# Kernel optimization log

Measured on AMD Instinct MI355X. Metric: run time of the kernel, lower is better.

The kernel has to match this reference:

```python
import jax, jax.numpy as jnp
import numpy as np

N = 50000
LEAKY_SLOPE = 0.2


def gat_layer(x, src, dst, W, a_src, a_dst, bias, concat):
    """PyG-style GATConv (eval mode, self-loops already in src/dst).
    x: [N, Fin]; W: [Fin, H*C]; a_src, a_dst: [H, C]; bias: [H*C] or [C].
    """
    H, C = a_src.shape
    h = (x @ W).reshape(-1, H, C)                      # [N, H, C]
    alpha_src = jnp.einsum('nhc,hc->nh', h, a_src)      # [N, H]
    alpha_dst = jnp.einsum('nhc,hc->nh', h, a_dst)      # [N, H]
    e = jax.nn.leaky_relu(alpha_src[src] + alpha_dst[dst], LEAKY_SLOPE)  # [E, H]
    # scatter-softmax over incoming edges of each destination node
    m = jax.lax.stop_gradient(jax.ops.segment_max(e, dst, num_segments=N))
    e = jnp.exp(e - m[dst])
    denom = jax.ops.segment_sum(e, dst, num_segments=N)  # [N, H]
    alpha = e / (denom[dst] + 1e-16)                     # [E, H]
    msg = h[src] * alpha[:, :, None]                     # [E, H, C]
    out = jax.ops.segment_sum(msg, dst, num_segments=N)  # [N, H, C]
    out = out.reshape(-1, H * C) if concat else out.mean(axis=1)
    return out + bias


def setup_inputs() -> dict:
    key = jax.random.key(0)
    ks = jax.random.split(key, 10)
    Fin, Hd, Hh = 256, 64, 4
    E = 1600000
    x = jax.random.normal(ks[0], (N, Fin), dtype=jnp.float32)
    edge_index = jax.random.randint(ks[1], (2, E), 0, N, dtype=jnp.int64)
    s = 1.0 / np.sqrt(Fin)
    W1 = jax.random.normal(ks[2], (Fin, Hh * Hd), dtype=jnp.float32) * s
    att_src1 = jax.random.normal(ks[3], (Hh, Hd), dtype=jnp.float32) * (1.0 / np.sqrt(Hd))
    att_dst1 = jax.random.normal(ks[4], (Hh, Hd), dtype=jnp.float32) * (1.0 / np.sqrt(Hd))
    b1 = jnp.zeros((Hh * Hd,), dtype=jnp.float32)
    W2 = jax.random.normal(ks[5], (Hh * Hd, Hd), dtype=jnp.float32) * (1.0 / np.sqrt(Hh * Hd))
    att_src2 = jax.random.normal(ks[6], (1, Hd), dtype=jnp.float32) * (1.0 / np.sqrt(Hd))
    att_dst2 = jax.random.normal(ks[7], (1, Hd), dtype=jnp.float32) * (1.0 / np.sqrt(Hd))
    b2 = jnp.zeros((Hd,), dtype=jnp.float32)
    return {"x": x, "edge_index": edge_index, "W1": W1, "att_src1": att_src1,
            "att_dst1": att_dst1, "b1": b1, "W2": W2, "att_src2": att_src2,
            "att_dst2": att_dst2, "b2": b2}


def reference(x, edge_index, W1, att_src1, att_dst1, b1, W2, att_src2, att_dst2, b2):
    # PyG GATConv adds self-loops by default
    loop = jnp.arange(N, dtype=edge_index.dtype)
    src = jnp.concatenate([edge_index[0], loop])
    dst = jnp.concatenate([edge_index[1], loop])
    h = gat_layer(x, src, dst, W1, att_src1, att_dst1, b1, concat=True)
    h = jax.nn.elu(h)            # dropout is identity in eval mode
    out = gat_layer(h, src, dst, W2, att_src2, att_dst2, b2, concat=False)
    return out
```

## Files before the change

### kernel.cpp

```cpp
#include <hip/hip_runtime.h>


typedef __attribute__((ext_vector_type(8))) short short8;
typedef __attribute__((ext_vector_type(4))) float floatx4;

#define FIN 256
#define H1 4
#define CH 64
#define CAP 16384

__device__ __forceinline__ float bf2f(ushort u) {
    union { unsigned int i; float f; } v; v.i = ((unsigned int)u) << 16; return v.f;
}
__device__ __forceinline__ ushort f2bf(float f) {
    union { float f; unsigned int i; } v; v.f = f;
    unsigned int r = v.i + 0x7fffu + ((v.i >> 16) & 1u);
    return (ushort)(r >> 16);
}
__device__ __forceinline__ float load_in(const void* p, int i, int f) {
    return f ? ((const float*)p)[i] : bf2f(((const ushort*)p)[i]);
}
__device__ __forceinline__ int load_idx(const void* p, long long i, int f64) {
    return f64 ? (int)((const long long*)p)[i] : ((const int*)p)[i];
}

__global__ __launch_bounds__(256) void probe_kernel(const ushort* __restrict__ x,
                                                    const int* __restrict__ ei,
                                                    int* __restrict__ flags,
                                                    int* __restrict__ bcnt) {
    __shared__ int s_nan, s_odd;
    int t = threadIdx.x;
    bcnt[t] = 0;
    if (t == 0) { s_nan = 0; s_odd = 0; }
    __syncthreads();
    int nanc = 0, oddc = 0;
    for (int i = t; i < 16384; i += 256) {
        ushort u = x[i];
        if (((u >> 7) & 0xFF) == 0xFF) nanc++;
    }
    for (int i = t; i < 2048; i += 256)
        if (ei[2 * i + 1] != 0) oddc++;
    if (nanc) atomicAdd(&s_nan, nanc);
    if (oddc) atomicAdd(&s_odd, oddc);
    __syncthreads();
    if (t == 0) {
        flags[0] = (s_nan >= 2) ? 1 : 0;
        flags[1] = (s_odd == 0) ? 1 : 0;
    }
}

__global__ __launch_bounds__(256) void prep_bucket_kernel(
        const void* __restrict__ x, const void* __restrict__ W1,
        const void* __restrict__ W2, ushort* __restrict__ xb,
        ushort* __restrict__ Wt1, ushort* __restrict__ Wt2,
        const void* __restrict__ ei, int* __restrict__ bcnt,
        unsigned int* __restrict__ buckets,
        int E, int Etot, int Nn, const int* __restrict__ flags,
        int PB_conv, int PB_tr_end) {
    __shared__ int lcnt[256], lbase[256], lcur[256];
    int bid = blockIdx.x, t = threadIdx.x;
    int f = flags[0];
    if (bid < PB_conv) {
        int i0 = bid * 2048 + t * 8;
        if (f) {
            float4 v0 = ((const float4*)x)[i0 / 4];
            float4 v1 = ((const float4*)x)[i0 / 4 + 1];
            ushort4 o0, o1;
            o0.x = f2bf(v0.x); o0.y = f2bf(v0.y); o0.z = f2bf(v0.z); o0.w = f2bf(v0.w);
            o1.x = f2bf(v1.x); o1.y = f2bf(v1.y); o1.z = f2bf(v1.z); o1.w = f2bf(v1.w);
            *(ushort4*)(xb + i0) = o0;
            *(ushort4*)(xb + i0 + 4) = o1;
        } else {
            *(uint4*)(xb + i0) = ((const uint4*)x)[i0 / 8];
        }
        return;
    }
    if (bid < PB_tr_end) {
        int j = (bid - PB_conv) * 256 + t;
        if (j < FIN * FIN) {
            int n = j / FIN, k = j % FIN;
            Wt1[j] = f2bf(load_in(W1, k * FIN + n, f));
        } else {
            int jj = j - FIN * FIN;
            int n = jj / FIN, k = jj % FIN;
            Wt2[jj] = f2bf(load_in(W2, k * CH + n, f));
        }
        return;
    }
    lcnt[t] = 0; lcur[t] = 0;
    __syncthreads();
    int f64 = flags[1];
    int base = (bid - PB_tr_end) * 4096 + t;
    unsigned int val[16]; int bk[16]; bool ok[16];
#pragma unroll
    for (int j = 0; j < 16; ++j) {
        int e = base + j * 256;
        ok[j] = e < Etot;
        bk[j] = 0; val[j] = 0;
        if (ok[j]) {
            int s, d;
            if (e < E) {
                s = load_idx(ei, e, f64);
                d = load_idx(ei, (long long)E + e, f64);
            } else {
                s = d = e - E;
            }
            s = min(max(s, 0), Nn - 1);
            d = min(max(d, 0), Nn - 1);
            bk[j] = d >> 8;
            val[j] = ((unsigned int)s << 8) | (unsigned int)(d & 255);
            atomicAdd(&lcnt[bk[j]], 1);
        }
    }
    __syncthreads();
    if (lcnt[t] > 0) lbase[t] = atomicAdd(&bcnt[t], lcnt[t]);
    __syncthreads();
#pragma unroll
    for (int j = 0; j < 16; ++j) {
        if (ok[j]) {
            int p = lbase[bk[j]] + atomicAdd(&lcur[bk[j]], 1);
            if (p < CAP) buckets[(size_t)bk[j] * CAP + p] = val[j];
        }
    }
}

__device__ __forceinline__ void gemm_core(const ushort* __restrict__ A,
                                          const ushort* __restrict__ Bt,
                                          ushort* __restrict__ C,
                                          int M, int K, int Nc,
                                          const void* __restrict__ aS,
                                          const void* __restrict__ aD,
                                          float* __restrict__ alphaS,
                                          float* __restrict__ alphaD,
                                          int H, int f, int gx, int head,
                                          int planar) {
    int tid = threadIdx.x;
    int wave = tid >> 6, lane = tid & 63, quad = lane >> 4, l16 = lane & 15;
    int rbase = gx * 256 + wave * 64;
    int cbase = head * 64;
    floatx4 acc[4][4];
#pragma unroll
    for (int i = 0; i < 4; i++)
#pragma unroll
        for (int j = 0; j < 4; j++) acc[i][j] = (floatx4)0.f;

    for (int kb = 0; kb < K; kb += 32) {
        int k0 = kb + quad * 8;
        short8 a[4], b[4];
#pragma unroll
        for (int mt = 0; mt < 4; mt++) {
            int row = rbase + mt * 16 + l16;
            if (row >= M) row = M - 1;
            a[mt] = *reinterpret_cast<const short8*>(A + (size_t)row * K + k0);
        }
#pragma unroll
        for (int nt = 0; nt < 4; nt++) {
            int col = cbase + nt * 16 + l16;
            b[nt] = *reinterpret_cast<const short8*>(Bt + (size_t)col * K + k0);
        }
#pragma unroll
        for (int mt = 0; mt < 4; mt++)
#pragma unroll
            for (int nt = 0; nt < 4; nt++)
                acc[mt][nt] = __builtin_amdgcn_mfma_f32_16x16x32_bf16(
                    a[mt], b[nt], acc[mt][nt], 0, 0, 0);
    }
    float asv[4], adv[4];
#pragma unroll
    for (int nt = 0; nt < 4; nt++) {
        int col = cbase + nt * 16 + l16;
        asv[nt] = load_in(aS, col, f);
        adv[nt] = load_in(aD, col, f);
    }
#pragma unroll
    for (int mt = 0; mt < 4; mt++) {
#pragma unroll
        for (int r = 0; r < 4; r++) {
            int row = rbase + mt * 16 + quad * 4 + r;
            float ps = 0.f, pd = 0.f;
#pragma unroll
            for (int nt = 0; nt < 4; nt++) {
                float w = acc[mt][nt][r];
                ps += w * asv[nt];
                pd += w * adv[nt];
            }
#pragma unroll
            for (int off = 8; off > 0; off >>= 1) {
                ps += __shfl_xor(ps, off, 16);
                pd += __shfl_xor(pd, off, 16);
            }
            if (row < M) {
                if (l16 == 0) {
                    alphaS[row * H + head] = ps;
                    alphaD[row * H + head] = pd;
                }
#pragma unroll
                for (int nt = 0; nt < 4; nt++) {
                    int col = cbase + nt * 16 + l16;
                    size_t caddr = planar
                        ? ((size_t)(col >> 7) * M + row) * 128 + (col & 127)
                        : (size_t)row * Nc + col;
                    C[caddr] = f2bf(acc[mt][nt][r]);
                }
            }
        }
    }
}

__global__ __launch_bounds__(256) void gemm1_pass2_kernel(
        const ushort* __restrict__ A, const ushort* __restrict__ Bt,
        ushort* __restrict__ C, int M, int K, int Nc,
        const void* __restrict__ aS, const void* __restrict__ aD,
        float* __restrict__ alphaS, float* __restrict__ alphaD,
        const int* __restrict__ flags, int g1, int nbx,
        const int* __restrict__ bcnt, const unsigned int* __restrict__ buckets,
        int* __restrict__ offs, int* __restrict__ csr_src, int Nn) {
    __shared__ int part[256], sc[256], cur[256];
    int bid = blockIdx.x;
    int t = threadIdx.x;
    if (bid < g1) {
        gemm_core(A, Bt, C, M, K, Nc, aS, aD, alphaS, alphaD, 4, flags[0],
                  bid % nbx, bid / nbx, 1);
        return;
    }
    int b = bid - g1;
    part[t] = bcnt[t];
    __syncthreads();
#pragma unroll
    for (int off = 1; off < 256; off <<= 1) {
        int v = (t >= off) ? part[t - off] : 0;
        __syncthreads();
        part[t] += v;
        __syncthreads();
    }
    int basepos = (b == 0) ? 0 : part[b - 1];
    int nEdges = min(bcnt[b], CAP);
    sc[t] = 0;
    __syncthreads();
    const unsigned int* bk = buckets + (size_t)b * CAP;
    for (int i = t; i < nEdges; i += 256)
        atomicAdd(&sc[bk[i] & 255], 1);
    __syncthreads();
    int mycount = sc[t];
    __syncthreads();
#pragma unroll
    for (int off = 1; off < 256; off <<= 1) {
        int v = (t >= off) ? sc[t - off] : 0;
        __syncthreads();
        sc[t] += v;
        __syncthreads();
    }
    int excl = sc[t] - mycount;
    int gnode = b * 256 + t;
    if (gnode <= Nn) offs[gnode] = basepos + excl;
    cur[t] = excl;
    __syncthreads();
    for (int i = t; i < nEdges; i += 256) {
        unsigned int v = bk[i];
        int p = atomicAdd(&cur[v & 255], 1);
        csr_src[basepos + p] = (int)(v >> 8);
    }
}

__global__ __launch_bounds__(256) void gemm2_kernel(const ushort* __restrict__ A,
                                                    const ushort* __restrict__ Bt,
                                                    ushort* __restrict__ C,
                                                    int M, int K, int Nc,
                                                    const void* __restrict__ aS,
                                                    const void* __restrict__ aD,
                                                    float* __restrict__ alphaS,
                                                    float* __restrict__ alphaD,
                                                    const int* __restrict__ flags) {
    gemm_core(A, Bt, C, M, K, Nc, aS, aD, alphaS, alphaD, 1, flags[0],
              blockIdx.x, blockIdx.y, 0);
}

__global__ __launch_bounds__(256) void gat_node1_pass(
        const int* __restrict__ csr_src, const int* __restrict__ offs,
        const float* __restrict__ asrc, const float* __restrict__ adst,
        const ushort* __restrict__ h1p, const void* __restrict__ b1,
        ushort* __restrict__ hmidb, int Nn, const int* __restrict__ flags,
        int plane) {
    int f = flags[0];
    int wave = threadIdx.x >> 6, lane = threadIdx.x & 63;
    int n = blockIdx.x * 4 + wave;
    if (n >= Nn) return;
    int half = lane >> 5, l5 = lane & 31;
    int head = plane * 2 + (l5 >> 4);
    float ad = adst[n * H1 + head];
    unsigned rowoff = (unsigned)(plane * Nn) * 128u + (unsigned)l5 * 4u;
    int beg = offs[n], end = offs[n + 1];
    float a0 = 0.f, a1 = 0.f, a2 = 0.f, a3 = 0.f, l = 0.f;

    int e = beg;
    while (e + 16 <= end) {
        int sj[8]; float aj[8]; uint2 vj[8];
#pragma unroll
        for (int j = 0; j < 8; ++j) sj[j] = csr_src[e + 2 * j + half];
#pragma unroll
        for (int j = 0; j < 8; ++j) {
            aj[j] = asrc[sj[j] * H1 + head];
            vj[j] = *(const uint2*)(h1p + rowoff + (unsigned)sj[j] * 128u);
        }
#pragma unroll
        for (int j = 0; j < 8; ++j) {
            float s = aj[j] + ad;
            s = fmaxf(s, 0.2f * s);
            float p = __expf(s);
            l += p;
            union { unsigned int i; float fl; } c0, c1, c2, c3;
            c0.i = vj[j].x << 16; c1.i = vj[j].x & 0xffff0000u;
            c2.i = vj[j].y << 16; c3.i = vj[j].y & 0xffff0000u;
            a0 += p * c0.fl; a1 += p * c1.fl;
            a2 += p * c2.fl; a3 += p * c3.fl;
        }
        e += 16;
    }
    if (e < end) {
        int sj[8]; float aj[8]; uint2 vj[8];
#pragma unroll
        for (int j = 0; j < 8; ++j) {
            int ei = e + 2 * j + half;
            sj[j] = csr_src[ei < end ? ei : beg];
        }
#pragma unroll
        for (int j = 0; j < 8; ++j) {
            int ei = e + 2 * j + half;
            aj[j] = (ei < end) ? asrc[sj[j] * H1 + head] : -1e30f;
            vj[j] = *(const uint2*)(h1p + rowoff + (unsigned)sj[j] * 128u);
        }
#pragma unroll
        for (int j = 0; j < 8; ++j) {
            float s = aj[j] + ad;
            s = fmaxf(s, 0.2f * s);
            float p = __expf(s);
            l += p;
            union { unsigned int i; float fl; } c0, c1, c2, c3;
            c0.i = vj[j].x << 16; c1.i = vj[j].x & 0xffff0000u;
            c2.i = vj[j].y << 16; c3.i = vj[j].y & 0xffff0000u;
            a0 += p * c0.fl; a1 += p * c1.fl;
            a2 += p * c2.fl; a3 += p * c3.fl;
        }
    }
    a0 += __shfl_xor(a0, 32); a1 += __shfl_xor(a1, 32);
    a2 += __shfl_xor(a2, 32); a3 += __shfl_xor(a3, 32);
    l  += __shfl_xor(l, 32);
    if (half == 0) {
        float inv = 1.f / (l + 1e-16f);
        int cb = plane * 128 + l5 * 4;
        float o0 = a0 * inv + load_in(b1, cb + 0, f);
        float o1 = a1 * inv + load_in(b1, cb + 1, f);
        float o2 = a2 * inv + load_in(b1, cb + 2, f);
        float o3 = a3 * inv + load_in(b1, cb + 3, f);
        o0 = o0 > 0.f ? o0 : __expf(o0) - 1.f;
        o1 = o1 > 0.f ? o1 : __expf(o1) - 1.f;
        o2 = o2 > 0.f ? o2 : __expf(o2) - 1.f;
        o3 = o3 > 0.f ? o3 : __expf(o3) - 1.f;
        uint2 st;
        st.x = (unsigned int)f2bf(o0) | ((unsigned int)f2bf(o1) << 16);
        st.y = (unsigned int)f2bf(o2) | ((unsigned int)f2bf(o3) << 16);
        *(uint2*)(hmidb + (unsigned)n * 256u + (unsigned)cb) = st;
    }
}

__global__ __launch_bounds__(256) void gat_node2(const int* __restrict__ csr_src,
                                                 const int* __restrict__ offs,
                                                 const float* __restrict__ asrc,
                                                 const float* __restrict__ adst,
                                                 const ushort* __restrict__ h2b,
                                                 const void* __restrict__ b2,
                                                 void* __restrict__ out, int Nn,
                                                 const int* __restrict__ flags) {
    int f = flags[0];
    int wave = threadIdx.x >> 6, lane = threadIdx.x & 63;
    int n = blockIdx.x * 4 + wave;
    if (n >= Nn) return;
    int q = lane >> 4, l4 = lane & 15;
    float ad = adst[n];
    int beg = offs[n], end = offs[n + 1];
    float a0 = 0.f, a1 = 0.f, a2 = 0.f, a3 = 0.f, l = 0.f;

    int e = beg;
    while (e + 16 <= end) {
        int sj[4]; float aj[4]; uint2 vj[4];
#pragma unroll
        for (int j = 0; j < 4; ++j) sj[j] = csr_src[e + 4 * j + q];
#pragma unroll
        for (int j = 0; j < 4; ++j) {
            aj[j] = asrc[sj[j]];
            vj[j] = *(const uint2*)(h2b + (unsigned)sj[j] * 64u + (unsigned)l4 * 4u);
        }
#pragma unroll
        for (int j = 0; j < 4; ++j) {
            float s = aj[j] + ad;
            s = fmaxf(s, 0.2f * s);
            float p = __expf(s);
            l += p;
            union { unsigned int i; float fl; } c0, c1, c2, c3;
            c0.i = vj[j].x << 16; c1.i = vj[j].x & 0xffff0000u;
            c2.i = vj[j].y << 16; c3.i = vj[j].y & 0xffff0000u;
            a0 += p * c0.fl; a1 += p * c1.fl;
            a2 += p * c2.fl; a3 += p * c3.fl;
        }
        e += 16;
    }
    if (e < end) {
        int sj[4]; float aj[4]; uint2 vj[4];
#pragma unroll
        for (int j = 0; j < 4; ++j) {
            int ei = e + 4 * j + q;
            sj[j] = csr_src[ei < end ? ei : beg];
        }
#pragma unroll
        for (int j = 0; j < 4; ++j) {
            int ei = e + 4 * j + q;
            aj[j] = (ei < end) ? asrc[sj[j]] : -1e30f;
            vj[j] = *(const uint2*)(h2b + (unsigned)sj[j] * 64u + (unsigned)l4 * 4u);
        }
#pragma unroll
        for (int j = 0; j < 4; ++j) {
            float s = aj[j] + ad;
            s = fmaxf(s, 0.2f * s);
            float p = __expf(s);
            l += p;
            union { unsigned int i; float fl; } c0, c1, c2, c3;
            c0.i = vj[j].x << 16; c1.i = vj[j].x & 0xffff0000u;
            c2.i = vj[j].y << 16; c3.i = vj[j].y & 0xffff0000u;
            a0 += p * c0.fl; a1 += p * c1.fl;
            a2 += p * c2.fl; a3 += p * c3.fl;
        }
    }
#pragma unroll
    for (int off = 16; off <= 32; off <<= 1) {
        a0 += __shfl_xor(a0, off); a1 += __shfl_xor(a1, off);
        a2 += __shfl_xor(a2, off); a3 += __shfl_xor(a3, off);
        l  += __shfl_xor(l, off);
    }
    if (lane < 16) {
        float inv = 1.f / (l + 1e-16f);
        float o0 = a0 * inv + load_in(b2, l4 * 4 + 0, f);
        float o1 = a1 * inv + load_in(b2, l4 * 4 + 1, f);
        float o2 = a2 * inv + load_in(b2, l4 * 4 + 2, f);
        float o3 = a3 * inv + load_in(b2, l4 * 4 + 3, f);
        if (f) {
            float4 st; st.x = o0; st.y = o1; st.z = o2; st.w = o3;
            *(float4*)((float*)out + (unsigned)n * 64u + (unsigned)l4 * 4u) = st;
        } else {
            uint2 st;
            st.x = (unsigned int)f2bf(o0) | ((unsigned int)f2bf(o1) << 16);
            st.y = (unsigned int)f2bf(o2) | ((unsigned int)f2bf(o3) << 16);
            *(uint2*)((ushort*)out + (unsigned)n * 64u + (unsigned)l4 * 4u) = st;
        }
    }
}

extern "C" void kernel_launch(void* const* d_in, const int* in_sizes, int n_in,
                              void* d_out, int out_size, void* d_ws, size_t ws_size,
                              hipStream_t stream) {
    const void* x   = d_in[0];
    const void* ei  = d_in[1];
    const void* W1  = d_in[2];
    const void* as1 = d_in[3];
    const void* ad1 = d_in[4];
    const void* b1  = d_in[5];
    const void* W2  = d_in[6];
    const void* as2 = d_in[7];
    const void* ad2 = d_in[8];
    const void* b2  = d_in[9];

    const int Nn = in_sizes[0] / FIN;
    const int E  = in_sizes[1] / 2;
    const int ET = E + Nn;
    const int NB = (Nn + 255) >> 8;

    char* ws = (char*)d_ws;
    size_t off = 0;
    auto alloc = [&](size_t bytes) {
        size_t o = off;
        off += (bytes + 255) & ~(size_t)255;
        return o;
    };
    ushort* xb    = (ushort*)(ws + alloc((size_t)Nn * FIN * 2));
    ushort* h1b   = (ushort*)(ws + alloc((size_t)Nn * FIN * 2));
    ushort* hmidb = (ushort*)(ws + alloc((size_t)Nn * FIN * 2));
    ushort* h2b   = (ushort*)(ws + alloc((size_t)Nn * CH * 2));
    ushort* Wt1   = (ushort*)(ws + alloc((size_t)FIN * FIN * 2));
    ushort* Wt2   = (ushort*)(ws + alloc((size_t)CH * FIN * 2));
    float* as1f   = (float*)(ws + alloc((size_t)Nn * H1 * 4));
    float* ad1f   = (float*)(ws + alloc((size_t)Nn * H1 * 4));
    float* as2f   = (float*)(ws + alloc((size_t)Nn * 4));
    float* ad2f   = (float*)(ws + alloc((size_t)Nn * 4));
    int*   offs   = (int*)(ws + alloc((size_t)(Nn + 1) * 4));
    int*   csr    = (int*)(ws + alloc((size_t)ET * 4));
    unsigned int* buckets = (unsigned int*)(ws + alloc((size_t)256 * CAP * 4));
    int*   bcnt   = (int*)(ws + alloc(256 * 4));
    int*   flags  = (int*)(ws + alloc(256));
    (void)ws_size; (void)n_in; (void)out_size;

    probe_kernel<<<1, 256, 0, stream>>>((const ushort*)x, (const int*)ei, flags, bcnt);

    int PB_conv = (Nn * FIN) / 2048;
    int PB_tr   = (FIN * FIN + CH * FIN) / 256;
    int PB_bkt  = (ET + 4095) / 4096;
    prep_bucket_kernel<<<PB_conv + PB_tr + PB_bkt, 256, 0, stream>>>(
        x, W1, W2, xb, Wt1, Wt2, ei, bcnt, buckets,
        E, ET, Nn, flags, PB_conv, PB_conv + PB_tr);

    int nbx = (Nn + 255) / 256;
    int g1 = nbx * H1;
    gemm1_pass2_kernel<<<g1 + NB, 256, 0, stream>>>(
        xb, Wt1, h1b, Nn, FIN, FIN, as1, ad1, as1f, ad1f,
        flags, g1, nbx, bcnt, buckets, offs, csr, Nn);

    gat_node1_pass<<<(Nn + 3) / 4, 256, 0, stream>>>(
        csr, offs, as1f, ad1f, h1b, b1, hmidb, Nn, flags, 0);
    gat_node1_pass<<<(Nn + 3) / 4, 256, 0, stream>>>(
        csr, offs, as1f, ad1f, h1b, b1, hmidb, Nn, flags, 1);

    gemm2_kernel<<<dim3((Nn + 255) / 256, 1), 256, 0, stream>>>(
        hmidb, Wt2, h2b, Nn, FIN, CH, as2, ad2, as2f, ad2f, flags);
    gat_node2<<<(Nn + 3) / 4, 256, 0, stream>>>(csr, offs, as2f, ad2f, h2b, b2, d_out, Nn, flags);
}
```

Baseline: 364.6 us.

## Remap edge aggregation lanes to 8 edges per wave with wide row loads

Both node aggregation kernels now split each wave into 8 edge slots of 8 lanes. Each lane loads 16 or 8 bf16 channels with uint4 loads and accumulates with packed float2 math, where it used to load 4 channels with uint2 loads. This cuts the number of per-edge index and attention-score loads and exp evaluations per lane, and aims for better memory-level parallelism on the gather. The cost is more accumulator registers and a longer cross-lane shuffle reduction with three xor stages over more values. Each loop iteration also keeps fewer independent gathers in flight.

After: 361.6 us. No clear change (-0.8%).

```diff
diff --git a/kernel.cpp b/kernel.cpp
--- a/kernel.cpp
+++ b/kernel.cpp
@@ -3,6 +3,7 @@
 
 typedef __attribute__((ext_vector_type(8))) short short8;
 typedef __attribute__((ext_vector_type(4))) float floatx4;
+typedef __attribute__((ext_vector_type(2))) float fx2;
 
 #define FIN 256
 #define H1 4
@@ -22,6 +23,38 @@
 }
 __device__ __forceinline__ int load_idx(const void* p, long long i, int f64) {
     return f64 ? (int)((const long long*)p)[i] : ((const int*)p)[i];
+}
+
+__device__ __forceinline__ float edge_p(float s) {
+    s = fmaxf(s, 0.2f * s);
+    return __expf(s);
+}
+
+__device__ __forceinline__ void accum16(fx2* acc, uint4 v0, uint4 v1,
+                                        float p, float& l) {
+    l += p;
+    fx2 pv = {p, p};
+    unsigned w[8] = {v0.x, v0.y, v0.z, v0.w, v1.x, v1.y, v1.z, v1.w};
+#pragma unroll
+    for (int u = 0; u < 8; ++u) {
+        union { unsigned i; float fl; } lo, hi;
+        lo.i = w[u] << 16; hi.i = w[u] & 0xffff0000u;
+        fx2 c = {lo.fl, hi.fl};
+        acc[u] += pv * c;
+    }
+}
+
+__device__ __forceinline__ void accum8(fx2* acc, uint4 v, float p, float& l) {
+    l += p;
+    fx2 pv = {p, p};
+    unsigned w[4] = {v.x, v.y, v.z, v.w};
+#pragma unroll
+    for (int u = 0; u < 4; ++u) {
+        union { unsigned i; float fl; } lo, hi;
+        lo.i = w[u] << 16; hi.i = w[u] & 0xffff0000u;
+        fx2 c = {lo.fl, hi.fl};
+        acc[u] += pv * c;
+    }
 }
 
 __global__ __launch_bounds__(256) void probe_kernel(const ushort* __restrict__ x,
@@ -285,81 +318,74 @@
     int wave = threadIdx.x >> 6, lane = threadIdx.x & 63;
     int n = blockIdx.x * 4 + wave;
     if (n >= Nn) return;
-    int half = lane >> 5, l5 = lane & 31;
-    int head = plane * 2 + (l5 >> 4);
+    int slot = lane >> 3, cg = lane & 7;
+    int head = plane * 2 + (cg >> 2);
     float ad = adst[n * H1 + head];
-    unsigned rowoff = (unsigned)(plane * Nn) * 128u + (unsigned)l5 * 4u;
+    unsigned rowbase = (unsigned)(plane * Nn) * 128u + (unsigned)cg * 16u;
     int beg = offs[n], end = offs[n + 1];
-    float a0 = 0.f, a1 = 0.f, a2 = 0.f, a3 = 0.f, l = 0.f;
+    fx2 acc[8];
+#pragma unroll
+    for (int u = 0; u < 8; ++u) acc[u] = (fx2)0.f;
+    float l = 0.f;
 
     int e = beg;
     while (e + 16 <= end) {
-        int sj[8]; float aj[8]; uint2 vj[8];
-#pragma unroll
-        for (int j = 0; j < 8; ++j) sj[j] = csr_src[e + 2 * j + half];
-#pragma unroll
-        for (int j = 0; j < 8; ++j) {
-            aj[j] = asrc[sj[j] * H1 + head];
-            vj[j] = *(const uint2*)(h1p + rowoff + (unsigned)sj[j] * 128u);
-        }
-#pragma unroll
-        for (int j = 0; j < 8; ++j) {
-            float s = aj[j] + ad;
-            s = fmaxf(s, 0.2f * s);
-            float p = __expf(s);
-            l += p;
-            union { unsigned int i; float fl; } c0, c1, c2, c3;
-            c0.i = vj[j].x << 16; c1.i = vj[j].x & 0xffff0000u;
-            c2.i = vj[j].y << 16; c3.i = vj[j].y & 0xffff0000u;
-            a0 += p * c0.fl; a1 += p * c1.fl;
-            a2 += p * c2.fl; a3 += p * c3.fl;
-        }
+        int sa = csr_src[e + slot];
+        int sb = csr_src[e + 8 + slot];
+        float aa = asrc[sa * H1 + head];
+        float ab = asrc[sb * H1 + head];
+        const uint4* ra = (const uint4*)(h1p + rowbase + (unsigned)sa * 128u);
+        const uint4* rb = (const uint4*)(h1p + rowbase + (unsigned)sb * 128u);
+        uint4 va0 = ra[0], va1 = ra[1];
+        uint4 vb0 = rb[0], vb1 = rb[1];
+        float pa = edge_p(aa + ad);
+        float pb = edge_p(ab + ad);
+        accum16(acc, va0, va1, pa, l);
+        accum16(acc, vb0, vb1, pb, l);
         e += 16;
     }
     if (e < end) {
-        int sj[8]; float aj[8]; uint2 vj[8];
-#pragma unroll
-        for (int j = 0; j < 8; ++j) {
-            int ei = e + 2 * j + half;
-            sj[j] = csr_src[ei < end ? ei : beg];
-        }
-#pragma unroll
-        for (int j = 0; j < 8; ++j) {
-            int ei = e + 2 * j + half;
-            aj[j] = (ei < end) ? asrc[sj[j] * H1 + head] : -1e30f;
-            vj[j] = *(const uint2*)(h1p + rowoff + (unsigned)sj[j] * 128u);
-        }
-#pragma unroll
-        for (int j = 0; j < 8; ++j) {
-            float s = aj[j] + ad;
-            s = fmaxf(s, 0.2f * s);
-            float p = __expf(s);
-            l += p;
-            union { unsigned int i; float fl; } c0, c1, c2, c3;
-            c0.i = vj[j].x << 16; c1.i = vj[j].x & 0xffff0000u;
-            c2.i = vj[j].y << 16; c3.i = vj[j].y & 0xffff0000u;
-            a0 += p * c0.fl; a1 += p * c1.fl;
-            a2 += p * c2.fl; a3 += p * c3.fl;
-        }
-    }
-    a0 += __shfl_xor(a0, 32); a1 += __shfl_xor(a1, 32);
-    a2 += __shfl_xor(a2, 32); a3 += __shfl_xor(a3, 32);
-    l  += __shfl_xor(l, 32);
-    if (half == 0) {
+        int ea = e + slot, eb = e + 8 + slot;
+        bool oka = ea < end, okb = eb < end;
+        int sa = csr_src[oka ? ea : beg];
+        int sb = csr_src[okb ? eb : beg];
+        float aa = asrc[sa * H1 + head];
+        float ab = asrc[sb * H1 + head];
+        const uint4* ra = (const uint4*)(h1p + rowbase + (unsigned)sa * 128u);
+        const uint4* rb = (const uint4*)(h1p + rowbase + (unsigned)sb * 128u);
+        uint4 va0 = ra[0], va1 = ra[1];
+        uint4 vb0 = rb[0], vb1 = rb[1];
+        float pa = edge_p(oka ? aa + ad : -1e30f);
+        float pb = edge_p(okb ? ab + ad : -1e30f);
+        accum16(acc, va0, va1, pa, l);
+        accum16(acc, vb0, vb1, pb, l);
+    }
+#pragma unroll
+    for (int off = 8; off <= 32; off <<= 1) {
+#pragma unroll
+        for (int u = 0; u < 8; ++u) {
+            acc[u][0] += __shfl_xor(acc[u][0], off);
+            acc[u][1] += __shfl_xor(acc[u][1], off);
+        }
+        l += __shfl_xor(l, off);
+    }
+    if (slot == 0) {
         float inv = 1.f / (l + 1e-16f);
-        int cb = plane * 128 + l5 * 4;
-        float o0 = a0 * inv + load_in(b1, cb + 0, f);
-        float o1 = a1 * inv + load_in(b1, cb + 1, f);
-        float o2 = a2 * inv + load_in(b1, cb + 2, f);
-        float o3 = a3 * inv + load_in(b1, cb + 3, f);
-        o0 = o0 > 0.f ? o0 : __expf(o0) - 1.f;
-        o1 = o1 > 0.f ? o1 : __expf(o1) - 1.f;
-        o2 = o2 > 0.f ? o2 : __expf(o2) - 1.f;
-        o3 = o3 > 0.f ? o3 : __expf(o3) - 1.f;
-        uint2 st;
-        st.x = (unsigned int)f2bf(o0) | ((unsigned int)f2bf(o1) << 16);
-        st.y = (unsigned int)f2bf(o2) | ((unsigned int)f2bf(o3) << 16);
-        *(uint2*)(hmidb + (unsigned)n * 256u + (unsigned)cb) = st;
+        int cb = plane * 128 + cg * 16;
+        unsigned ow[8];
+#pragma unroll
+        for (int u = 0; u < 8; ++u) {
+            float o0 = acc[u][0] * inv + load_in(b1, cb + 2 * u, f);
+            float o1 = acc[u][1] * inv + load_in(b1, cb + 2 * u + 1, f);
+            o0 = o0 > 0.f ? o0 : __expf(o0) - 1.f;
+            o1 = o1 > 0.f ? o1 : __expf(o1) - 1.f;
+            ow[u] = (unsigned)f2bf(o0) | ((unsigned)f2bf(o1) << 16);
+        }
+        uint4 st0, st1;
+        st0.x = ow[0]; st0.y = ow[1]; st0.z = ow[2]; st0.w = ow[3];
+        st1.x = ow[4]; st1.y = ow[5]; st1.z = ow[6]; st1.w = ow[7];
+        uint4* dst = (uint4*)(hmidb + (unsigned)n * 256u + (unsigned)cb);
+        dst[0] = st0; dst[1] = st1;
     }
 }
 
@@ -375,81 +401,74 @@
     int wave = threadIdx.x >> 6, lane = threadIdx.x & 63;
     int n = blockIdx.x * 4 + wave;
     if (n >= Nn) return;
-    int q = lane >> 4, l4 = lane & 15;
+    int slot = lane >> 3, cg = lane & 7;
     float ad = adst[n];
+    unsigned rowoff = (unsigned)cg * 8u;
     int beg = offs[n], end = offs[n + 1];
-    float a0 = 0.f, a1 = 0.f, a2 = 0.f, a3 = 0.f, l = 0.f;
+    fx2 acc[4];
+#pragma unroll
+    for (int u = 0; u < 4; ++u) acc[u] = (fx2)0.f;
+    float l = 0.f;
 
     int e = beg;
     while (e + 16 <= end) {
-        int sj[4]; float aj[4]; uint2 vj[4];
-#pragma unroll
-        for (int j = 0; j < 4; ++j) sj[j] = csr_src[e + 4 * j + q];
-#pragma unroll
-        for (int j = 0; j < 4; ++j) {
-            aj[j] = asrc[sj[j]];
-            vj[j] = *(const uint2*)(h2b + (unsigned)sj[j] * 64u + (unsigned)l4 * 4u);
-        }
-#pragma unroll
-        for (int j = 0; j < 4; ++j) {
-            float s = aj[j] + ad;
-            s = fmaxf(s, 0.2f * s);
-            float p = __expf(s);
-            l += p;
-            union { unsigned int i; float fl; } c0, c1, c2, c3;
-            c0.i = vj[j].x << 16; c1.i = vj[j].x & 0xffff0000u;
-            c2.i = vj[j].y << 16; c3.i = vj[j].y & 0xffff0000u;
-            a0 += p * c0.fl; a1 += p * c1.fl;
-            a2 += p * c2.fl; a3 += p * c3.fl;
-        }
+        int sa = csr_src[e + slot];
+        int sb = csr_src[e + 8 + slot];
+        float aa = asrc[sa];
+        float ab = asrc[sb];
+        uint4 va = *(const uint4*)(h2b + rowoff + (unsigned)sa * 64u);
+        uint4 vb = *(const uint4*)(h2b + rowoff + (unsigned)sb * 64u);
+        float pa = edge_p(aa + ad);
+        float pb = edge_p(ab + ad);
+        accum8(acc, va, pa, l);
+        accum8(acc, vb, pb, l);
         e += 16;
     }
     if (e < end) {
-        int sj[4]; float aj[4]; uint2 vj[4];
-#pragma unroll
-        for (int j = 0; j < 4; ++j) {
-            int ei = e + 4 * j + q;
-            sj[j] = csr_src[ei < end ? ei : beg];
-        }
-#pragma unroll
-        for (int j = 0; j < 4; ++j) {
-            int ei = e + 4 * j + q;
-            aj[j] = (ei < end) ? asrc[sj[j]] : -1e30f;
-            vj[j] = *(const uint2*)(h2b + (unsigned)sj[j] * 64u + (unsigned)l4 * 4u);
-        }
-#pragma unroll
-        for (int j = 0; j < 4; ++j) {
-            float s = aj[j] + ad;
-            s = fmaxf(s, 0.2f * s);
-            float p = __expf(s);
-            l += p;
-            union { unsigned int i; float fl; } c0, c1, c2, c3;
-            c0.i = vj[j].x << 16; c1.i = vj[j].x & 0xffff0000u;
-            c2.i = vj[j].y << 16; c3.i = vj[j].y & 0xffff0000u;
-            a0 += p * c0.fl; a1 += p * c1.fl;
-            a2 += p * c2.fl; a3 += p * c3.fl;
-        }
-    }
-#pragma unroll
-    for (int off = 16; off <= 32; off <<= 1) {
-        a0 += __shfl_xor(a0, off); a1 += __shfl_xor(a1, off);
-        a2 += __shfl_xor(a2, off); a3 += __shfl_xor(a3, off);
-        l  += __shfl_xor(l, off);
-    }
-    if (lane < 16) {
+        int ea = e + slot, eb = e + 8 + slot;
+        bool oka = ea < end, okb = eb < end;
+        int sa = csr_src[oka ? ea : beg];
+        int sb = csr_src[okb ? eb : beg];
+        float aa = asrc[sa];
+        float ab = asrc[sb];
+        uint4 va = *(const uint4*)(h2b + rowoff + (unsigned)sa * 64u);
+        uint4 vb = *(const uint4*)(h2b + rowoff + (unsigned)sb * 64u);
+        float pa = edge_p(oka ? aa + ad : -1e30f);
+        float pb = edge_p(okb ? ab + ad : -1e30f);
+        accum8(acc, va, pa, l);
+        accum8(acc, vb, pb, l);
+    }
+#pragma unroll
+    for (int off = 8; off <= 32; off <<= 1) {
+#pragma unroll
+        for (int u = 0; u < 4; ++u) {
+            acc[u][0] += __shfl_xor(acc[u][0], off);
+            acc[u][1] += __shfl_xor(acc[u][1], off);
+        }
+        l += __shfl_xor(l, off);
+    }
+    if (slot == 0) {
         float inv = 1.f / (l + 1e-16f);
-        float o0 = a0 * inv + load_in(b2, l4 * 4 + 0, f);
-        float o1 = a1 * inv + load_in(b2, l4 * 4 + 1, f);
-        float o2 = a2 * inv + load_in(b2, l4 * 4 + 2, f);
-        float o3 = a3 * inv + load_in(b2, l4 * 4 + 3, f);
+        float o[8];
+#pragma unroll
+        for (int u = 0; u < 4; ++u) {
+            o[2 * u]     = acc[u][0] * inv + load_in(b2, cg * 8 + 2 * u, f);
+            o[2 * u + 1] = acc[u][1] * inv + load_in(b2, cg * 8 + 2 * u + 1, f);
+        }
         if (f) {
-            float4 st; st.x = o0; st.y = o1; st.z = o2; st.w = o3;
-            *(float4*)((float*)out + (unsigned)n * 64u + (unsigned)l4 * 4u) = st;
+            float* op = (float*)out + (unsigned)n * 64u + (unsigned)cg * 8u;
+            float4 s0, s1;
+            s0.x = o[0]; s0.y = o[1]; s0.z = o[2]; s0.w = o[3];
+            s1.x = o[4]; s1.y = o[5]; s1.z = o[6]; s1.w = o[7];
+            *(float4*)op = s0;
+            *(float4*)(op + 4) = s1;
         } else {
-            uint2 st;
-            st.x = (unsigned int)f2bf(o0) | ((unsigned int)f2bf(o1) << 16);
-            st.y = (unsigned int)f2bf(o2) | ((unsigned int)f2bf(o3) << 16);
-            *(uint2*)((ushort*)out + (unsigned)n * 64u + (unsigned)l4 * 4u) = st;
+            uint4 st;
+            st.x = (unsigned)f2bf(o[0]) | ((unsigned)f2bf(o[1]) << 16);
+            st.y = (unsigned)f2bf(o[2]) | ((unsigned)f2bf(o[3]) << 16);
+            st.z = (unsigned)f2bf(o[4]) | ((unsigned)f2bf(o[5]) << 16);
+            st.w = (unsigned)f2bf(o[6]) | ((unsigned)f2bf(o[7]) << 16);
+            *(uint4*)((ushort*)out + (unsigned)n * 64u + (unsigned)cg * 8u) = st;
         }
     }
 }
```
